# Kernel tuning notes

Measured on AMD Instinct MI355X. Metric: run time of the kernel, lower is better.

## Reference

```python
import jax, jax.numpy as jnp
import numpy as np

B, L = 32, 96
N = B * L
E = B * L * L
HID, LAT, EEMB = 128, 64, 32
NLAYERS = 3
LAMBDA_CONTRAST = 0.05


def _sinusoidal(t, dim):
    half = dim // 2
    freqs = jnp.exp(-jnp.log(10000.0) * jnp.arange(half, dtype=jnp.float32) / (half - 1))
    ang = t[:, None] * freqs[None, :]
    return jnp.concatenate([jnp.sin(ang), jnp.cos(ang)], axis=-1)


def _forward(H_0, X_0, H_1, X_1, cond_embedding, t_graph,
             Wi1, bi1, Wi2, bi2, Wi3, bi3, edge_table,
             We1, be1, We2, be2, Wx, Wh1, bh1, Wh2, bh2, Wout, bout,
             edges, chain_ids, generate_mask, lengths, shift):
    n = H_0.shape[0]
    b = lengths.shape[0]
    batch_ids = jnp.repeat(jnp.arange(b), lengths, total_repeat_length=n)
    t = t_graph[batch_ids]                      # (N,)
    mask = generate_mask
    mask_f = mask.astype(jnp.float32)

    # path interpolation
    tH = t[:, None]
    H_t = jnp.where(mask[:, None], (1.0 - tH) * H_0 + tH * H_1, H_1)
    X_t = jnp.where(mask[:, None], (1.0 - tH) * X_0 + tH * X_1, X_1)
    v_H_target = H_1 - H_0
    v_X_target = X_1 - X_0

    # edge types from chain-id masking (irregular gather)
    row, col = edges[0], edges[1]
    edge_types = (chain_ids[row] != chain_ids[col]).astype(jnp.int32)

    # --- velocity net ---
    t_embed = _sinusoidal(t, HID)
    h = jnp.concatenate([H_t, cond_embedding, t_embed], axis=-1)
    h = jax.nn.relu(h @ Wi1 + bi1)
    h = jax.nn.relu(h @ Wi2 + bi2)
    h = h @ Wi3 + bi3                            # (N, HID)
    eemb = edge_table[edge_types]                # (E, EEMB)

    X = X_t
    for l in range(NLAYERS):
        rel = X[row] - X[col]                    # (E, 3)
        d2 = jnp.sum(rel * rel, axis=-1, keepdims=True)
        ef = jnp.concatenate([h[row], h[col], d2, eemb], axis=-1)
        m = jax.nn.silu(ef @ We1[l] + be1[l])
        m = jax.nn.silu(m @ We2[l] + be2[l])     # (E, HID)
        coef = m @ Wx[l]                         # (E, 1)
        X = X + jax.ops.segment_sum(rel * coef, row, num_segments=n)
        agg = jax.ops.segment_sum(m, row, num_segments=n)
        hh = jnp.concatenate([h, agg], axis=-1)
        h = h + jax.nn.silu(hh @ Wh1[l] + bh1[l]) @ Wh2[l] + bh2[l]

    v_X_pred = jnp.where(mask[:, None], X, 0.0)
    v_H_pred = jnp.where(mask[:, None], h @ Wout + bout, 0.0)

    # --- losses ---
    msum = mask_f.sum() + 1e-8
    def masked_mse(pred, tgt):
        return (jnp.sum((pred - tgt) ** 2, axis=-1) * mask_f).sum() / msum
    loss_H_pos = masked_mse(v_H_pred, v_H_target)
    loss_X_pos = masked_mse(v_X_pred, v_X_target)

    # negatives: roll over node dim (matches torch indexing (arange+shift)%N)
    v_H_target_neg = jnp.roll(H_1, -shift, axis=0) - jnp.roll(H_0, -shift, axis=0)
    v_X_target_neg = jnp.roll(X_1, -shift, axis=0) - jnp.roll(X_0, -shift, axis=0)
    loss_H_neg = masked_mse(v_H_pred, v_H_target_neg)
    loss_X_neg = masked_mse(v_X_pred, v_X_target_neg)

    loss_H = loss_H_pos - LAMBDA_CONTRAST * loss_H_neg
    loss_X = loss_X_pos - LAMBDA_CONTRAST * loss_X_neg
    return jnp.stack([loss_H, loss_X, loss_H_pos, loss_X_pos, loss_H_neg, loss_X_neg])


def setup_inputs() -> dict:
    key = jax.random.key(0)
    ks = iter(jax.random.split(key, 40))
    def nrm(shape, fan_in):
        return jax.random.normal(next(ks), shape, dtype=jnp.float32) / np.sqrt(fan_in)

    # all-pairs edges within each graph (uniform lengths)
    idx = np.arange(L)
    rb, cb = np.repeat(idx, L), np.tile(idx, L)
    off = (np.arange(B) * L)[:, None]
    rows = (off + rb[None, :]).reshape(-1)
    cols = (off + cb[None, :]).reshape(-1)
    edges = jnp.asarray(np.stack([rows, cols]).astype(np.int32))

    d_in_mlp = LAT + 2 * HID       # 320
    d_in_e = 2 * HID + 1 + EEMB    # 289
    inp = {
        "H_0": jax.random.normal(next(ks), (N, LAT), dtype=jnp.float32),
        "X_0": jax.random.normal(next(ks), (N, 3), dtype=jnp.float32),
        "H_1": jax.random.normal(next(ks), (N, LAT), dtype=jnp.float32),
        "X_1": jax.random.normal(next(ks), (N, 3), dtype=jnp.float32),
        "cond_embedding": jax.random.normal(next(ks), (N, HID), dtype=jnp.float32),
        "t_graph": jax.random.uniform(next(ks), (B,), dtype=jnp.float32),
        "Wi1": nrm((d_in_mlp, HID), d_in_mlp), "bi1": jnp.zeros((HID,)),
        "Wi2": nrm((HID, HID), HID), "bi2": jnp.zeros((HID,)),
        "Wi3": nrm((HID, HID), HID), "bi3": jnp.zeros((HID,)),
        "edge_table": jax.random.normal(next(ks), (2, EEMB), dtype=jnp.float32),
        "We1": nrm((NLAYERS, d_in_e, HID), d_in_e), "be1": jnp.zeros((NLAYERS, HID)),
        "We2": nrm((NLAYERS, HID, HID), HID), "be2": jnp.zeros((NLAYERS, HID)),
        "Wx": nrm((NLAYERS, HID, 1), HID) * 0.01,
        "Wh1": nrm((NLAYERS, 2 * HID, HID), 2 * HID), "bh1": jnp.zeros((NLAYERS, HID)),
        "Wh2": nrm((NLAYERS, HID, HID), HID), "bh2": jnp.zeros((NLAYERS, HID)),
        "Wout": nrm((HID, LAT), HID), "bout": jnp.zeros((LAT,)),
        "edges": edges,
        "chain_ids": jax.random.randint(next(ks), (N,), 0, 3).astype(jnp.int32),
        "generate_mask": jax.random.bernoulli(next(ks), 0.5, (N,)),
        "lengths": jnp.full((B,), L, dtype=jnp.int32),
        "shift": 7,
    }
    return inp


def reference(H_0, X_0, H_1, X_1, cond_embedding, t_graph,
              Wi1, bi1, Wi2, bi2, Wi3, bi3, edge_table,
              We1, be1, We2, be2, Wx, Wh1, bh1, Wh2, bh2, Wout, bout,
              edges, chain_ids, generate_mask, lengths, shift):
    return _forward(H_0, X_0, H_1, X_1, cond_embedding, t_graph,
                    Wi1, bi1, Wi2, bi2, Wi3, bi3, edge_table,
                    We1, be1, We2, be2, Wx, Wh1, bh1, Wh2, bh2, Wout, bout,
                    edges, chain_ids, generate_mask, lengths, shift)
```

## Files before the change

kernel.cpp:

```cpp
#include <hip/hip_runtime.h>
#include <hip/hip_bf16.h>
#include <math.h>

#define NBATCH 32
#define LSEQ   96
#define NN     3072
#define HID    128
#define LAT    64
#define EEMB   32

#define OFF_H      0
#define OFF_X      (OFF_H   + NN*HID)
#define OFF_PA     (OFF_X   + NN*3)
#define OFF_AGG    (OFF_PA  + NN*HID)
#define OFF_DX     (OFF_AGG + NN*HID)
#define OFF_ET     (OFF_DX  + NN*3)
#define OFF_ACC    (OFF_ET  + 768)
#define OFF_NBID   (OFF_ACC + 8)
#define OFF_CUM    (OFF_NBID + NN)
#define OFF_PBH    (OFF_CUM + 40)
#define OFF_BPE    (OFF_PBH + NN*HID/2)
#define OFF_BAB    (OFF_BPE + 24576)
#define OFF_BH1    (OFF_BAB + 49152)
#define OFF_BH2    (OFF_BH1 + 49152)
#define OFF_BWO    (OFF_BH2 + 24576)
#define OFF_BWI1   (OFF_BWO + 4096)
#define OFF_BWI2   (OFF_BWI1 + 20480)
#define OFF_BWI3   (OFF_BWI2 + 8192)
#define OFF_CNT    (OFF_BWI3 + 8192)

typedef short bf16x8 __attribute__((ext_vector_type(8)));
typedef float f32x4  __attribute__((ext_vector_type(4)));

__device__ __forceinline__ short f2bf(float f) {
    unsigned u = __builtin_bit_cast(unsigned, f);
    unsigned r = (u + 0x7FFFu + ((u >> 16) & 1u)) >> 16;
    return (short)r;
}
__device__ __forceinline__ short2 f2bf2(float a, float b) {
    __hip_bfloat162 h = __float22bfloat162_rn(make_float2(a, b));
    short2 r;
    __builtin_memcpy(&r, &h, sizeof(r));
    return r;
}
__device__ __forceinline__ float bf2f(short s) {
    unsigned u = ((unsigned)(unsigned short)s) << 16;
    return __builtin_bit_cast(float, u);
}
__device__ __forceinline__ float silu(float z) {
    return z * __builtin_amdgcn_rcpf(1.0f + __expf(-z));
}

__global__ void k0_all(const float* __restrict__ edge_table, const float* __restrict__ We1,
                       const int* __restrict__ lengths, const float* __restrict__ We2,
                       const float* __restrict__ Wh1, const float* __restrict__ Wh2,
                       const float* __restrict__ Wout, const float* __restrict__ Wi1,
                       const float* __restrict__ Wi2, const float* __restrict__ Wi3,
                       float* __restrict__ ws) {
    int tid = threadIdx.x;
    if (blockIdx.x == 1472) {
        int* cum = (int*)(ws + OFF_CUM);
        int* nb  = (int*)(ws + OFF_NBID);
        float* et = ws + OFF_ET;
        if (tid == 0) {
            int s = 0;
            for (int b = 0; b < NBATCH; b++) { cum[b] = s; s += lengths[b]; }
            cum[NBATCH] = s;
        }
        if (tid < 8) ws[OFF_ACC + tid] = 0.0f;
        if (tid < 128) ((unsigned*)(ws + OFF_CNT))[tid] = 0u;
        __syncthreads();
        for (int i = tid; i < NN; i += blockDim.x) {
            int b = NBATCH - 1;
            for (int q = 0; q < NBATCH; q++) { if (i < cum[q + 1]) { b = q; break; } }
            nb[i] = b;
        }
        for (int idx = tid; idx < 3 * 2 * HID; idx += blockDim.x) {
            int c = idx & 127;
            int t = (idx >> 7) & 1;
            int l = idx >> 8;
            const float* w = We1 + (l * 289 + 257) * HID + c;
            const float* e = edge_table + t * EEMB;
            float s = 0.f;
            for (int k = 0; k < EEMB; k++) s += e[k] * w[k * HID];
            et[idx] = s;
        }
        return;
    }
    int idx = blockIdx.x * 256 + tid;
    short* bpe  = (short*)(ws + OFF_BPE);
    short* bab  = (short*)(ws + OFF_BAB);
    short* bh1  = (short*)(ws + OFF_BH1);
    short* bh2  = (short*)(ws + OFF_BH2);
    short* bwo  = (short*)(ws + OFF_BWO);
    short* bwi1 = (short*)(ws + OFF_BWI1);
    short* bwi2 = (short*)(ws + OFF_BWI2);
    short* bwi3 = (short*)(ws + OFF_BWI3);
    if (idx < 49152) {
// ... 129 lines not shown
            acc[i] = __builtin_amdgcn_mfma_f32_16x16x32_bf16(af, bf, acc[i], 0, 0, 0);
        }
    }
    #pragma unroll
    for (int i = 0; i < 2; i++) {
        int ch = 16 * (2 * w + i) + lp;
        float bb2 = bi2[ch];
        #pragma unroll
        for (int r = 0; r < 4; r++)
            u2[(quad * 4 + r) * 136 + ch] = f2bf(fmaxf(acc[i][r] + bb2, 0.0f));
    }
    __syncthreads();

    acc[0] = (f32x4){0.f, 0.f, 0.f, 0.f};
    acc[1] = (f32x4){0.f, 0.f, 0.f, 0.f};
    #pragma unroll
    for (int s = 0; s < 4; s++) {
        int kb = s * 32 + quad * 8;
        bf16x8 af = *(const bf16x8*)(u2 + lp * 136 + kb);
        #pragma unroll
        for (int i = 0; i < 2; i++) {
            int ct = 2 * w + i;
            bf16x8 bf = *(const bf16x8*)(bwi3 + (size_t)(16 * ct + lp) * 128 + kb);
            acc[i] = __builtin_amdgcn_mfma_f32_16x16x32_bf16(af, bf, acc[i], 0, 0, 0);
        }
    }
    #pragma unroll
    for (int i = 0; i < 2; i++) {
        int ch = 16 * (2 * w + i) + lp;
        float bb3 = bi3[ch];
        #pragma unroll
        for (int r = 0; r < 4; r++) {
            int row = quad * 4 + r;
            float h = acc[i][r] + bb3;
            ws[OFF_H + (size_t)(rowbase + row) * 128 + ch] = h;
            u1[row * 136 + ch] = f2bf(h);
        }
    }
    __syncthreads();

    f32x4 acc4[4];
    #pragma unroll
    for (int i = 0; i < 4; i++) acc4[i] = (f32x4){0.f, 0.f, 0.f, 0.f};
    #pragma unroll
    for (int s = 0; s < 4; s++) {
        int kb = s * 32 + quad * 8;
        bf16x8 af = *(const bf16x8*)(u1 + lp * 136 + kb);
        #pragma unroll
        for (int i = 0; i < 4; i++) {
            int ct4 = 4 * w + i;
            bf16x8 bf = *(const bf16x8*)(bab + (size_t)(16 * ct4 + lp) * 128 + kb);
            acc4[i] = __builtin_amdgcn_mfma_f32_16x16x32_bf16(af, bf, acc4[i], 0, 0, 0);
        }
    }
    short* pbh = (short*)(ws + OFF_PBH);
    #pragma unroll
    for (int i = 0; i < 4; i++) {
        int ct4 = 4 * w + i;
        #pragma unroll
        for (int r = 0; r < 4; r++) {
            int node = rowbase + quad * 4 + r;
            if (ct4 < 8) {
                int ch = 16 * ct4 + lp;
                ws[OFF_PA + (size_t)node * 128 + ch] = acc4[i][r] + be1[ch];
            } else {
                int ch = 16 * (ct4 - 8) + lp;
                pbh[(size_t)node * 128 + ch] = f2bf(acc4[i][r]);
            }
        }
    }
}

#define KG 4
#define SMC_BS    0
#define SMC_AGG   32768
#define SMC_PE0   45056
#define SMC_PE1   47104
#define SMC_WC    49152
#define SMC_BE2   49664
#define SMC_WX    50176
#define SMC_COEF  50688
#define SMC_XT    52224
#define SMC_CI    52272
__global__ void __launch_bounds__(384)
k3v_edge(const float* __restrict__ We1, const float* __restrict__ Wx,
         const float* __restrict__ be2, const int* __restrict__ chain,
         int l, float* __restrict__ ws) {
    __shared__ __align__(16) char smem[52288];
    short* bS    = (short*)(smem + SMC_BS);
    float* aggP  = (float*)(smem + SMC_AGG);
    float* pe0S  = (float*)(smem + SMC_PE0);
    float* pe1S  = (float*)(smem + SMC_PE1);
    float* wcS   = (float*)(smem + SMC_WC);
    float* be2S  = (float*)(smem + SMC_BE2);
    float* wxS   = (float*)(smem + SMC_WX);
    float* coefS = (float*)(smem + SMC_COEF);
    float* xT    = (float*)(smem + SMC_XT);
    int*   ciS   = (int*)  (smem + SMC_CI);

    int tid = threadIdx.x;
    int i0 = blockIdx.x * KG;
    int colbase = (i0 / 96) * 96;
    const float* Xc = ws + OFF_X;

    {
        const short* bpe = (const short*)(ws + OFF_BPE) + (size_t)l * 128 * 128;
        for (int idx = tid; idx < 2048; idx += 384) {
            int t = idx >> 8, s = (idx >> 6) & 3, ln = idx & 63;
            int lq = ln >> 4, lpp = ln & 15;
            *(bf16x8*)(bS + idx * 8) =
                *(const bf16x8*)(bpe + (size_t)(16 * t + lpp) * 128 + s * 32 + lq * 8);
        }
        if (tid < 128) {
            float et0 = ws[OFF_ET + l * 256 + tid];
            float et1 = ws[OFF_ET + l * 256 + 128 + tid];
            #pragma unroll
            for (int g = 0; g < KG; g++) {
                float pav = ws[OFF_PA + (size_t)(i0 + g) * 128 + tid];
                pe0S[g * 128 + tid] = pav + et0;
                pe1S[g * 128 + tid] = pav + et1;
            }
            wcS[tid]  = We1[(l * 289 + 256) * 128 + tid];
            be2S[tid] = be2[l * 128 + tid];
            wxS[tid]  = Wx[l * 128 + tid];
        }
        if (tid < KG * 3) xT[tid] = Xc[(size_t)(i0 + tid / 3) * 3 + tid % 3];
        if (tid < KG) ciS[tid] = chain[i0 + tid];
    }

    int w = tid >> 6, lane = tid & 63;
    int quad = lane >> 4, lp = lane & 15;
    int jA = 16 * w + lp;
    const short* pbrow = (const short*)(ws + OFF_PBH) + (size_t)(colbase + jA) * 128;
    float xr0 = Xc[(size_t)(colbase + jA) * 3 + 0];
    float xr1 = Xc[(size_t)(colbase + jA) * 3 + 1];
    float xr2 = Xc[(size_t)(colbase + jA) * 3 + 2];
    int cj = chain[colbase + jA];
    float ex0 = 0.f, ex1 = 0.f;
    if (w < 3) {
        ex0 = Xc[(size_t)(colbase + lane) * 3 + w];
        if (lane < 32) ex1 = Xc[(size_t)(colbase + lane + 64) * 3 + w];
    }
    __syncthreads();

    #pragma unroll
    for (int gr = 0; gr < 2; gr++) {
        int g0 = 2 * gr, g1 = 2 * gr + 1;
        float rx0 = xT[g0 * 3 + 0] - xr0, ry0 = xT[g0 * 3 + 1] - xr1, rz0 = xT[g0 * 3 + 2] - xr2;
        float rx1 = xT[g1 * 3 + 0] - xr0, ry1 = xT[g1 * 3 + 1] - xr1, rz1 = xT[g1 * 3 + 2] - xr2;
        float d20 = rx0 * rx0 + ry0 * ry0 + rz0 * rz0;
        float d21 = rx1 * rx1 + ry1 * ry1 + rz1 * rz1;
        const float* peB0 = ((cj != ciS[g0]) ? pe1S : pe0S) + g0 * 128;
        const float* peB1 = ((cj != ciS[g1]) ? pe1S : pe0S) + g1 * 128;

        bf16x8 af0[4], af1[4];
        #pragma unroll
        for (int s = 0; s < 4; s++) {
            int kb = s * 32 + quad * 8;
            bf16x8 pb = *(const bf16x8*)(pbrow + kb);
            float4 w0 = *(const float4*)(wcS + kb);
            float4 w1 = *(const float4*)(wcS + kb + 4);
            float wcv[8] = {w0.x, w0.y, w0.z, w0.w, w1.x, w1.y, w1.z, w1.w};
            float4 pa0 = *(const float4*)(peB0 + kb);
            float4 pa1 = *(const float4*)(peB0 + kb + 4);
            float4 pb0 = *(const float4*)(peB1 + kb);
            float4 pb1 = *(const float4*)(peB1 + kb + 4);
            float pe0v[8] = {pa0.x, pa0.y, pa0.z, pa0.w, pa1.x, pa1.y, pa1.z, pa1.w};
            float pe1v[8] = {pb0.x, pb0.y, pb0.z, pb0.w, pb1.x, pb1.y, pb1.z, pb1.w};
            float z0[8], z1[8];
            #pragma unroll
            for (int e = 0; e < 8; e++) {
                float pbf = bf2f(pb[e]);
                z0[e] = silu(pe0v[e] + pbf + d20 * wcv[e]);
                z1[e] = silu(pe1v[e] + pbf + d21 * wcv[e]);
            }
            #pragma unroll
            for (int e = 0; e < 8; e += 2) {
                short2 p0 = f2bf2(z0[e], z0[e + 1]);
                short2 p1 = f2bf2(z1[e], z1[e + 1]);
                af0[s][e] = p0.x; af0[s][e + 1] = p0.y;
                af1[s][e] = p1.x; af1[s][e + 1] = p1.y;
            }
        }

        float cp0[4] = {0.f, 0.f, 0.f, 0.f};
        float cp1[4] = {0.f, 0.f, 0.f, 0.f};
        #pragma unroll
        for (int t = 0; t < 8; t++) {
            f32x4 a0 = (f32x4){0.f, 0.f, 0.f, 0.f};
            f32x4 a1 = (f32x4){0.f, 0.f, 0.f, 0.f};
            #pragma unroll
            for (int s = 0; s < 4; s++) {
                bf16x8 bf = *(const bf16x8*)(bS + ((t * 4 + s) * 64 + lane) * 8);
                a0 = __builtin_amdgcn_mfma_f32_16x16x32_bf16(af0[s], bf, a0, 0, 0, 0);
                a1 = __builtin_amdgcn_mfma_f32_16x16x32_bf16(af1[s], bf, a1, 0, 0, 0);
            }
            float be2v = be2S[16 * t + lp];
            float wxv  = wxS[16 * t + lp];
            float ag0 = 0.f, ag1 = 0.f;
            #pragma unroll
            for (int r = 0; r < 4; r++) {
                float m20 = silu(a0[r] + be2v);
                float m21 = silu(a1[r] + be2v);
                ag0 += m20; ag1 += m21;
                cp0[r] += m20 * wxv;
                cp1[r] += m21 * wxv;
            }
            ag0 += __shfl_xor(ag0, 16); ag0 += __shfl_xor(ag0, 32);
            ag1 += __shfl_xor(ag1, 16); ag1 += __shfl_xor(ag1, 32);
            if (lane < 16) {
                aggP[(g0 * 6 + w) * 128 + 16 * t + lp] = ag0;
                aggP[(g1 * 6 + w) * 128 + 16 * t + lp] = ag1;
            }
        }
        #pragma unroll
        for (int r = 0; r < 4; r++) {
            float v0 = cp0[r], v1 = cp1[r];
            v0 += __shfl_xor(v0, 1); v1 += __shfl_xor(v1, 1);
            v0 += __shfl_xor(v0, 2); v1 += __shfl_xor(v1, 2);
            v0 += __shfl_xor(v0, 4); v1 += __shfl_xor(v1, 4);
            v0 += __shfl_xor(v0, 8); v1 += __shfl_xor(v1, 8);
            if (lp == 0) {
                coefS[g0 * 96 + 16 * w + quad * 4 + r] = v0;
                coefS[g1 * 96 + 16 * w + quad * 4 + r] = v1;
            }
        }
        __syncthreads();

        if (tid < 256) {
            int gg = tid >> 7, ch = tid & 127;
            int g = 2 * gr + gg;
            float s = 0.f;
            #pragma unroll
            for (int q = 0; q < 6; q++) s += aggP[(g * 6 + q) * 128 + ch];
            ws[OFF_AGG + (size_t)(i0 + g) * 128 + ch] = s;
        }
        if (w < 3) {
            #pragma unroll
            for (int gg = 0; gg < 2; gg++) {
                int g = 2 * gr + gg;
                float v = (xT[g * 3 + w] - ex0) * coefS[g * 96 + lane];
                if (lane < 32) v += (xT[g * 3 + w] - ex1) * coefS[g * 96 + lane + 64];
                #pragma unroll
                for (int o = 32; o > 0; o >>= 1) v += __shfl_down(v, o);
                if (lane == 0) ws[OFF_DX + (size_t)(i0 + g) * 3 + w] = v;
            }
        }
    }
}

__global__ void __launch_bounds__(256)
k4s_node_post(const float* __restrict__ bh1, const float* __restrict__ bh2,
              const float* __restrict__ be1, const float* __restrict__ bout,
              const float* __restrict__ H0, const float* __restrict__ X0,
              const float* __restrict__ H1, const float* __restrict__ X1,
              const int* __restrict__ gmask, const int* __restrict__ shiftp,
              int l, float* __restrict__ ws, float* __restrict__ out) {
    __shared__ short uS[16 * 136];
    __shared__ short hS[16 * 136];
    __shared__ float redE[4], redN[4];
    __shared__ float sxp, sxn, scnt;
    int rowbase = blockIdx.x * 96 + blockIdx.y * 16;
    int tid = threadIdx.x;
    int w = tid >> 6, lane = tid & 63;
    int quad = lane >> 4, lp = lane & 15;
    int nodeA = rowbase + lp;
    const short* b1 = (const short*)(ws + OFF_BH1) + (size_t)l * 128 * 256;
    const short* b2 = (const short*)(ws + OFF_BH2) + (size_t)l * 128 * 128;

    if (tid == 0) { sxp = 0.f; sxn = 0.f; scnt = 0.f; }
    if (tid < 48) {
        int node = rowbase + tid / 3, d = tid % 3;
        ws[OFF_X + (size_t)node * 3 + d] += ws[OFF_DX + (size_t)node * 3 + d];
    }

    f32x4 acc[2];
    acc[0] = (f32x4){0.f, 0.f, 0.f, 0.f};
    acc[1] = (f32x4){0.f, 0.f, 0.f, 0.f};
    #pragma unroll
    for (int s = 0; s < 8; s++) {
        int kb = s * 32 + quad * 8;
        const float* src = (kb < 128) ? (ws + OFF_H + (size_t)nodeA * 128 + kb)
                                      : (ws + OFF_AGG + (size_t)nodeA * 128 + (kb - 128));
        bf16x8 af;
        #pragma unroll
        for (int e = 0; e < 8; e += 2) {
            short2 p = f2bf2(src[e], src[e + 1]);
            af[e] = p.x; af[e + 1] = p.y;
        }
        #pragma unroll
        for (int i = 0; i < 2; i++) {
            int ct = 2 * w + i;
            bf16x8 bf = *(const bf16x8*)(b1 + (size_t)(16 * ct + lp) * 256 + kb);
            acc[i] = __builtin_amdgcn_mfma_f32_16x16x32_bf16(af, bf, acc[i], 0, 0, 0);
        }
    }
    #pragma unroll
    for (int i = 0; i < 2; i++) {
        int ch = 16 * (2 * w + i) + lp;
        float bb1 = bh1[l * 128 + ch];
        #pragma unroll
        for (int r = 0; r < 4; r++)
            uS[(quad * 4 + r) * 136 + ch] = f2bf(silu(acc[i][r] + bb1));
    }
    __syncthreads();

    acc[0] = (f32x4){0.f, 0.f, 0.f, 0.f};
    acc[1] = (f32x4){0.f, 0.f, 0.f, 0.f};
    #pragma unroll
    for (int s = 0; s < 4; s++) {
        int kb = s * 32 + quad * 8;
        bf16x8 af = *(const bf16x8*)(uS + lp * 136 + kb);
        #pragma unroll
        for (int i = 0; i < 2; i++) {
            int ct = 2 * w + i;
            bf16x8 bf = *(const bf16x8*)(b2 + (size_t)(16 * ct + lp) * 128 + kb);
            acc[i] = __builtin_amdgcn_mfma_f32_16x16x32_bf16(af, bf, acc[i], 0, 0, 0);
        }
    }
    #pragma unroll
    for (int i = 0; i < 2; i++) {
        int ch = 16 * (2 * w + i) + lp;
        float bb2 = bh2[l * 128 + ch];
        #pragma unroll
        for (int r = 0; r < 4; r++) {
            int row = quad * 4 + r;
            size_t off = OFF_H + (size_t)(rowbase + row) * 128 + ch;
            float h = ws[off] + acc[i][r] + bb2;
            ws[off] = h;
            hS[row * 136 + ch] = f2bf(h);
        }
    }
    __syncthreads();

    if (l < 2) {
        const short* bab = (const short*)(ws + OFF_BAB) + (size_t)(l + 1) * 256 * 128;
        f32x4 acc4[4];
        #pragma unroll
        for (int i = 0; i < 4; i++) acc4[i] = (f32x4){0.f, 0.f, 0.f, 0.f};
        #pragma unroll
        for (int s = 0; s < 4; s++) {
            int kb = s * 32 + quad * 8;
            bf16x8 af = *(const bf16x8*)(hS + lp * 136 + kb);
            #pragma unroll
            for (int i = 0; i < 4; i++) {
                int ct4 = 4 * w + i;
                bf16x8 bf = *(const bf16x8*)(bab + (size_t)(16 * ct4 + lp) * 128 + kb);
                acc4[i] = __builtin_amdgcn_mfma_f32_16x16x32_bf16(af, bf, acc4[i], 0, 0, 0);
            }
        }
        short* pbh = (short*)(ws + OFF_PBH);
        #pragma unroll
        for (int i = 0; i < 4; i++) {
            int ct4 = 4 * w + i;
            #pragma unroll
            for (int r = 0; r < 4; r++) {
                int node = rowbase + quad * 4 + r;
                if (ct4 < 8) {
                    int ch = 16 * ct4 + lp;
                    ws[OFF_PA + (size_t)node * 128 + ch] = acc4[i][r] + be1[(l + 1) * 128 + ch];
                } else {
                    int ch = 16 * (ct4 - 8) + lp;
                    pbh[(size_t)node * 128 + ch] = f2bf(acc4[i][r]);
                }
            }
        }
    } else {
        const short* bwo = (const short*)(ws + OFF_BWO);
        f32x4 accv = (f32x4){0.f, 0.f, 0.f, 0.f};
        #pragma unroll
        for (int s = 0; s < 4; s++) {
            int kb = s * 32 + quad * 8;
            bf16x8 af = *(const bf16x8*)(hS + lp * 136 + kb);
            bf16x8 bf = *(const bf16x8*)(bwo + (size_t)(16 * w + lp) * 128 + kb);
            accv = __builtin_amdgcn_mfma_f32_16x16x32_bf16(af, bf, accv, 0, 0, 0);
        }
        int s = shiftp[0] % NN; if (s < 0) s += NN;
        int col = 16 * w + lp;
        float bo = bout[col];
        float ep = 0.f, en = 0.f;
        #pragma unroll
        for (int r = 0; r < 4; r++) {
            int row = rowbase + quad * 4 + r;
            if (gmask[row] != 0) {
                int ip = row + s; if (ip >= NN) ip -= NN;
                float v  = accv[r] + bo;
                float tp = H1[(size_t)row * 64 + col] - H0[(size_t)row * 64 + col];
                float tn = H1[(size_t)ip * 64 + col]  - H0[(size_t)ip * 64 + col];
                float dp = v - tp, dn = v - tn;
                ep += dp * dp;
                en += dn * dn;
            }
        }
        #pragma unroll
        for (int o = 1; o < 64; o <<= 1) {
            ep += __shfl_xor(ep, o);
            en += __shfl_xor(en, o);
        }
        if (lane == 0) { redE[w] = ep; redN[w] = en; }

        if (tid < 16) {
            int node = rowbase + tid;
            if (gmask[node] != 0) {
                int ip = node + s; if (ip >= NN) ip -= NN;
                float xp = 0.f, xn = 0.f;
                #pragma unroll
                for (int d = 0; d < 3; d++) {
                    float xv  = ws[OFF_X + (size_t)node * 3 + d];
                    float tpx = X1[(size_t)node * 3 + d] - X0[(size_t)node * 3 + d];
                    float tnx = X1[(size_t)ip * 3 + d]   - X0[(size_t)ip * 3 + d];
                    xp += (xv - tpx) * (xv - tpx);
                    xn += (xv - tnx) * (xv - tnx);
                }
                atomicAdd(&sxp, xp);
                atomicAdd(&sxn, xn);
                atomicAdd(&scnt, 1.0f);
            }
        }
        __syncthreads();
        if (tid == 0) {
            float eT = redE[0] + redE[1] + redE[2] + redE[3];
            float nT = redN[0] + redN[1] + redN[2] + redN[3];
            float* acc0 = ws + OFF_ACC;
            atomicAdd(acc0 + 0, eT);
            atomicAdd(acc0 + 2, nT);
            atomicAdd(acc0 + 1, sxp);
            atomicAdd(acc0 + 3, sxn);
            atomicAdd(acc0 + 4, scnt);
            __threadfence();
            unsigned o2 = atomicAdd((unsigned*)(ws + OFF_CNT) + 96, 1u);
            if (o2 == 191u) {
                __threadfence();
                float a0 = atomicAdd(acc0 + 0, 0.0f);
                float a1 = atomicAdd(acc0 + 1, 0.0f);
                float a2 = atomicAdd(acc0 + 2, 0.0f);
                float a3 = atomicAdd(acc0 + 3, 0.0f);
                float a4 = atomicAdd(acc0 + 4, 0.0f);
                float msum = a4 + 1e-8f;
                float lhp = a0 / msum, lxp = a1 / msum;
                float lhn = a2 / msum, lxn = a3 / msum;
                out[0] = lhp - 0.05f * lhn;
                out[1] = lxp - 0.05f * lxn;
                out[2] = lhp;
                out[3] = lxp;
                out[4] = lhn;
                out[5] = lxn;
            }
        }
    }
}

extern "C" void kernel_launch(void* const* d_in, const int* in_sizes, int n_in,
                              void* d_out, int out_size, void* d_ws, size_t ws_size,
                              hipStream_t stream) {
    (void)in_sizes; (void)n_in; (void)out_size; (void)ws_size;
    const float* H0   = (const float*)d_in[0];
    const float* X0   = (const float*)d_in[1];
    const float* H1   = (const float*)d_in[2];
    const float* X1   = (const float*)d_in[3];
    const float* cond = (const float*)d_in[4];
    const float* tg   = (const float*)d_in[5];
    const float* Wi1  = (const float*)d_in[6];
    const float* bi1  = (const float*)d_in[7];
    const float* Wi2  = (const float*)d_in[8];
    const float* bi2  = (const float*)d_in[9];
    const float* Wi3  = (const float*)d_in[10];
    const float* bi3  = (const float*)d_in[11];
    const float* etab = (const float*)d_in[12];
    const float* We1  = (const float*)d_in[13];
    const float* be1  = (const float*)d_in[14];
    const float* We2  = (const float*)d_in[15];
    const float* be2  = (const float*)d_in[16];
    const float* Wx   = (const float*)d_in[17];
    const float* Wh1  = (const float*)d_in[18];
    const float* bh1  = (const float*)d_in[19];
    const float* Wh2  = (const float*)d_in[20];
    const float* bh2  = (const float*)d_in[21];
    const float* Wout = (const float*)d_in[22];
    const float* bout = (const float*)d_in[23];
    const int* chain   = (const int*)d_in[25];
    const int* gmask   = (const int*)d_in[26];
    const int* lengths = (const int*)d_in[27];
    const int* shiftp  = (const int*)d_in[28];
    float* ws  = (float*)d_ws;
    float* out = (float*)d_out;

    k0_all<<<1473, 256, 0, stream>>>(etab, We1, lengths, We2, Wh1, Wh2,
                                     Wout, Wi1, Wi2, Wi3, ws);
    k1s_node_init<<<dim3(NBATCH, 6), 256, 0, stream>>>(H0, X0, H1, X1, cond, tg,
                                                       bi1, bi2, bi3, be1, gmask, ws);
    for (int l = 0; l < 3; l++) {
        k3v_edge<<<NN / KG, 384, 0, stream>>>(We1, Wx, be2, chain, l, ws);
        k4s_node_post<<<dim3(NBATCH, 6), 256, 0, stream>>>(bh1, bh2, be1, bout,
                                                           H0, X0, H1, X1, gmask, shiftp,
                                                           l, ws, out);
    }
}
```

Baseline: 353.5 us.

## Fuse edge message kernel with node update via ping-pong X and PBH buffers

Merges the per-layer edge kernel and the node post-processing kernel into one launch. Each 4-node block now reduces its aggregated messages in shared memory, applies the node MLP, and writes the next layer's projections itself. This removes the global agg buffer round trip and one launch per layer. Double-buffered X and bf16 projection buffers keep other blocks from reading values that are being overwritten. The cost is that node-MLP MFMAs use 16-row tiles with only 4 valid rows, and each of four times as many blocks re-reads the node weight matrices.

```diff
diff --git a/kernel.cpp b/kernel.cpp
--- a/kernel.cpp
+++ b/kernel.cpp
@@ -12,8 +12,8 @@
 #define OFF_H      0
 #define OFF_X      (OFF_H   + NN*HID)
 #define OFF_PA     (OFF_X   + NN*3)
-#define OFF_AGG    (OFF_PA  + NN*HID)
-#define OFF_DX     (OFF_AGG + NN*HID)
+#define OFF_PBH2   (OFF_PA  + NN*HID)
+#define OFF_DX     (OFF_PBH2 + NN*HID)
 #define OFF_ET     (OFF_DX  + NN*3)
 #define OFF_ACC    (OFF_ET  + 768)
 #define OFF_NBID   (OFF_ACC + 8)
@@ -309,11 +309,17 @@
 #define SMC_COEF  50688
 #define SMC_XT    52224
 #define SMC_CI    52272
+#define SMC_XN    52288
 __global__ void __launch_bounds__(384)
-k3v_edge(const float* __restrict__ We1, const float* __restrict__ Wx,
-         const float* __restrict__ be2, const int* __restrict__ chain,
-         int l, float* __restrict__ ws) {
-    __shared__ __align__(16) char smem[52288];
+k3f_edge_node(const float* __restrict__ We1, const float* __restrict__ Wx,
+              const float* __restrict__ be2, const int* __restrict__ chain,
+              const float* __restrict__ bh1, const float* __restrict__ bh2,
+              const float* __restrict__ be1, const float* __restrict__ bout,
+              const float* __restrict__ H0, const float* __restrict__ X0,
+              const float* __restrict__ H1, const float* __restrict__ X1,
+              const int* __restrict__ gmask, const int* __restrict__ shiftp,
+              int l, float* __restrict__ ws, float* __restrict__ out) {
+    __shared__ __align__(16) char smem[52336];
     short* bS    = (short*)(smem + SMC_BS);
     float* aggP  = (float*)(smem + SMC_AGG);
     float* pe0S  = (float*)(smem + SMC_PE0);
@@ -324,11 +330,15 @@
     float* coefS = (float*)(smem + SMC_COEF);
     float* xT    = (float*)(smem + SMC_XT);
     int*   ciS   = (int*)  (smem + SMC_CI);
+    float* xnS   = (float*)(smem + SMC_XN);
 
     int tid = threadIdx.x;
     int i0 = blockIdx.x * KG;
     int colbase = (i0 / 96) * 96;
-    const float* Xc = ws + OFF_X;
+    const float* Xin  = ws + ((l & 1) ? OFF_DX : OFF_X);
+    float*       Xout = ws + ((l & 1) ? OFF_X  : OFF_DX);
+    const short* pbh_in  = (const short*)(ws + ((l & 1) ? OFF_PBH2 : OFF_PBH));
+    short*       pbh_out = (short*)      (ws + ((l & 1) ? OFF_PBH  : OFF_PBH2));
 
     {
         const short* bpe = (const short*)(ws + OFF_BPE) + (size_t)l * 128 * 128;
@@ -351,22 +361,22 @@
             be2S[tid] = be2[l * 128 + tid];
             wxS[tid]  = Wx[l * 128 + tid];
         }
-        if (tid < KG * 3) xT[tid] = Xc[(size_t)(i0 + tid / 3) * 3 + tid % 3];
+        if (tid < KG * 3) xT[tid] = Xin[(size_t)(i0 + tid / 3) * 3 + tid % 3];
         if (tid < KG) ciS[tid] = chain[i0 + tid];
     }
 
     int w = tid >> 6, lane = tid & 63;
     int quad = lane >> 4, lp = lane & 15;
     int jA = 16 * w + lp;
-    const short* pbrow = (const short*)(ws + OFF_PBH) + (size_t)(colbase + jA) * 128;
-    float xr0 = Xc[(size_t)(colbase + jA) * 3 + 0];
-    float xr1 = Xc[(size_t)(colbase + jA) * 3 + 1];
-    float xr2 = Xc[(size_t)(colbase + jA) * 3 + 2];
+    const short* pbrow = pbh_in + (size_t)(colbase + jA) * 128;
+    float xr0 = Xin[(size_t)(colbase + jA) * 3 + 0];
+    float xr1 = Xin[(size_t)(colbase + jA) * 3 + 1];
+    float xr2 = Xin[(size_t)(colbase + jA) * 3 + 2];
     int cj = chain[colbase + jA];
     float ex0 = 0.f, ex1 = 0.f;
     if (w < 3) {
-        ex0 = Xc[(size_t)(colbase + lane) * 3 + w];
-        if (lane < 32) ex1 = Xc[(size_t)(colbase + lane + 64) * 3 + w];
+        ex0 = Xin[(size_t)(colbase + lane) * 3 + w];
+        if (lane < 32) ex1 = Xin[(size_t)(colbase + lane + 64) * 3 + w];
     }
     __syncthreads();
 
@@ -454,14 +464,6 @@
         }
         __syncthreads();
 
-        if (tid < 256) {
-            int gg = tid >> 7, ch = tid & 127;
-            int g = 2 * gr + gg;
-            float s = 0.f;
-            #pragma unroll
-            for (int q = 0; q < 6; q++) s += aggP[(g * 6 + q) * 128 + ch];
-            ws[OFF_AGG + (size_t)(i0 + g) * 128 + ch] = s;
-        }
         if (w < 3) {
             #pragma unroll
             for (int gg = 0; gg < 2; gg++) {
@@ -470,193 +472,180 @@
                 if (lane < 32) v += (xT[g * 3 + w] - ex1) * coefS[g * 96 + lane + 64];
                 #pragma unroll
                 for (int o = 32; o > 0; o >>= 1) v += __shfl_down(v, o);
-                if (lane == 0) ws[OFF_DX + (size_t)(i0 + g) * 3 + w] = v;
-            }
-        }
-    }
-}
-
-__global__ void __launch_bounds__(256)
-k4s_node_post(const float* __restrict__ bh1, const float* __restrict__ bh2,
-              const float* __restrict__ be1, const float* __restrict__ bout,
-              const float* __restrict__ H0, const float* __restrict__ X0,
-              const float* __restrict__ H1, const float* __restrict__ X1,
-              const int* __restrict__ gmask, const int* __restrict__ shiftp,
-              int l, float* __restrict__ ws, float* __restrict__ out) {
-    __shared__ short uS[16 * 136];
-    __shared__ short hS[16 * 136];
-    __shared__ float redE[4], redN[4];
-    __shared__ float sxp, sxn, scnt;
-    int rowbase = blockIdx.x * 96 + blockIdx.y * 16;
-    int tid = threadIdx.x;
-    int w = tid >> 6, lane = tid & 63;
-    int quad = lane >> 4, lp = lane & 15;
-    int nodeA = rowbase + lp;
-    const short* b1 = (const short*)(ws + OFF_BH1) + (size_t)l * 128 * 256;
-    const short* b2 = (const short*)(ws + OFF_BH2) + (size_t)l * 128 * 128;
-
-    if (tid == 0) { sxp = 0.f; sxn = 0.f; scnt = 0.f; }
-    if (tid < 48) {
-        int node = rowbase + tid / 3, d = tid % 3;
-        ws[OFF_X + (size_t)node * 3 + d] += ws[OFF_DX + (size_t)node * 3 + d];
-    }
-
-    f32x4 acc[2];
-    acc[0] = (f32x4){0.f, 0.f, 0.f, 0.f};
-    acc[1] = (f32x4){0.f, 0.f, 0.f, 0.f};
-    #pragma unroll
-    for (int s = 0; s < 8; s++) {
-        int kb = s * 32 + quad * 8;
-        const float* src = (kb < 128) ? (ws + OFF_H + (size_t)nodeA * 128 + kb)
-                                      : (ws + OFF_AGG + (size_t)nodeA * 128 + (kb - 128));
-        bf16x8 af;
-        #pragma unroll
-        for (int e = 0; e < 8; e += 2) {
-            short2 p = f2bf2(src[e], src[e + 1]);
-            af[e] = p.x; af[e + 1] = p.y;
-        }
-        #pragma unroll
-        for (int i = 0; i < 2; i++) {
-            int ct = 2 * w + i;
-            bf16x8 bf = *(const bf16x8*)(b1 + (size_t)(16 * ct + lp) * 256 + kb);
-            acc[i] = __builtin_amdgcn_mfma_f32_16x16x32_bf16(af, bf, acc[i], 0, 0, 0);
-        }
-    }
-    #pragma unroll
-    for (int i = 0; i < 2; i++) {
-        int ch = 16 * (2 * w + i) + lp;
-        float bb1 = bh1[l * 128 + ch];
-        #pragma unroll
-        for (int r = 0; r < 4; r++)
-            uS[(quad * 4 + r) * 136 + ch] = f2bf(silu(acc[i][r] + bb1));
-    }
+                if (lane == 0) {
+                    float xv = xT[g * 3 + w] + v;
+                    Xout[(size_t)(i0 + g) * 3 + w] = xv;
+                    xnS[g * 3 + w] = xv;
+                }
+            }
+        }
+    }
+
+    short* haggS = (short*)(smem + SMC_PE0);
+    short* uS    = (short*)(smem + SMC_COEF);
+    short* hS    = (short*)(smem + SMC_PE1);
+    const bf16x8 zf = (bf16x8){0, 0, 0, 0, 0, 0, 0, 0};
+
+    for (int idx = tid; idx < 1024; idx += 384) {
+        int g = idx >> 8, c = idx & 255;
+        float v;
+        if (c < 128) {
+            v = ws[OFF_H + (size_t)(i0 + g) * 128 + c];
+        } else {
+            int ch = c - 128;
+            v = 0.f;
+            #pragma unroll
+            for (int q = 0; q < 6; q++) v += aggP[(g * 6 + q) * 128 + ch];
+        }
+        haggS[g * 256 + c] = f2bf(v);
+    }
+    if (l == 2 && tid < 16) ((float*)(smem + SMC_WX))[tid] = 0.f;
     __syncthreads();
 
-    acc[0] = (f32x4){0.f, 0.f, 0.f, 0.f};
-    acc[1] = (f32x4){0.f, 0.f, 0.f, 0.f};
-    #pragma unroll
-    for (int s = 0; s < 4; s++) {
-        int kb = s * 32 + quad * 8;
-        bf16x8 af = *(const bf16x8*)(uS + lp * 136 + kb);
-        #pragma unroll
-        for (int i = 0; i < 2; i++) {
-            int ct = 2 * w + i;
-            bf16x8 bf = *(const bf16x8*)(b2 + (size_t)(16 * ct + lp) * 128 + kb);
-            acc[i] = __builtin_amdgcn_mfma_f32_16x16x32_bf16(af, bf, acc[i], 0, 0, 0);
-        }
-    }
-    #pragma unroll
-    for (int i = 0; i < 2; i++) {
-        int ch = 16 * (2 * w + i) + lp;
-        float bb2 = bh2[l * 128 + ch];
-        #pragma unroll
-        for (int r = 0; r < 4; r++) {
-            int row = quad * 4 + r;
-            size_t off = OFF_H + (size_t)(rowbase + row) * 128 + ch;
-            float h = ws[off] + acc[i][r] + bb2;
-            ws[off] = h;
-            hS[row * 136 + ch] = f2bf(h);
+    {
+        const short* b1 = (const short*)(ws + OFF_BH1) + (size_t)l * 128 * 256;
+        for (int ct = w; ct < 8; ct += 6) {
+            f32x4 acc = (f32x4){0.f, 0.f, 0.f, 0.f};
+            #pragma unroll
+            for (int s = 0; s < 8; s++) {
+                int kb = s * 32 + quad * 8;
+                bf16x8 af = zf;
+                if (lp < 4) af = *(const bf16x8*)(haggS + lp * 256 + kb);
+                bf16x8 bf = *(const bf16x8*)(b1 + (size_t)(16 * ct + lp) * 256 + kb);
+                acc = __builtin_amdgcn_mfma_f32_16x16x32_bf16(af, bf, acc, 0, 0, 0);
+            }
+            if (quad == 0) {
+                int ch = 16 * ct + lp;
+                float bb = bh1[l * 128 + ch];
+                #pragma unroll
+                for (int r = 0; r < 4; r++)
+                    uS[r * 136 + ch] = f2bf(silu(acc[r] + bb));
+            }
+        }
+    }
+    __syncthreads();
+
+    {
+        const short* b2 = (const short*)(ws + OFF_BH2) + (size_t)l * 128 * 128;
+        for (int ct = w; ct < 8; ct += 6) {
+            f32x4 acc = (f32x4){0.f, 0.f, 0.f, 0.f};
+            #pragma unroll
+            for (int s = 0; s < 4; s++) {
+                int kb = s * 32 + quad * 8;
+                bf16x8 af = zf;
+                if (lp < 4) af = *(const bf16x8*)(uS + lp * 136 + kb);
+                bf16x8 bf = *(const bf16x8*)(b2 + (size_t)(16 * ct + lp) * 128 + kb);
+                acc = __builtin_amdgcn_mfma_f32_16x16x32_bf16(af, bf, acc, 0, 0, 0);
+            }
+            if (quad == 0) {
+                int ch = 16 * ct + lp;
+                float bb = bh2[l * 128 + ch];
+                #pragma unroll
+                for (int r = 0; r < 4; r++) {
+                    size_t off = OFF_H + (size_t)(i0 + r) * 128 + ch;
+                    float h = ws[off] + acc[r] + bb;
+                    ws[off] = h;
+                    hS[r * 136 + ch] = f2bf(h);
+                }
+            }
         }
     }
     __syncthreads();
 
     if (l < 2) {
         const short* bab = (const short*)(ws + OFF_BAB) + (size_t)(l + 1) * 256 * 128;
-        f32x4 acc4[4];
-        #pragma unroll
-        for (int i = 0; i < 4; i++) acc4[i] = (f32x4){0.f, 0.f, 0.f, 0.f};
-        #pragma unroll
-        for (int s = 0; s < 4; s++) {
-            int kb = s * 32 + quad * 8;
-            bf16x8 af = *(const bf16x8*)(hS + lp * 136 + kb);
-            #pragma unroll
-            for (int i = 0; i < 4; i++) {
-                int ct4 = 4 * w + i;
+        for (int ct4 = w; ct4 < 16; ct4 += 6) {
+            f32x4 acc = (f32x4){0.f, 0.f, 0.f, 0.f};
+            #pragma unroll
+            for (int s = 0; s < 4; s++) {
+                int kb = s * 32 + quad * 8;
+                bf16x8 af = zf;
+                if (lp < 4) af = *(const bf16x8*)(hS + lp * 136 + kb);
                 bf16x8 bf = *(const bf16x8*)(bab + (size_t)(16 * ct4 + lp) * 128 + kb);
-                acc4[i] = __builtin_amdgcn_mfma_f32_16x16x32_bf16(af, bf, acc4[i], 0, 0, 0);
-            }
-        }
-        short* pbh = (short*)(ws + OFF_PBH);
-        #pragma unroll
-        for (int i = 0; i < 4; i++) {
-            int ct4 = 4 * w + i;
-            #pragma unroll
-            for (int r = 0; r < 4; r++) {
-                int node = rowbase + quad * 4 + r;
-                if (ct4 < 8) {
-                    int ch = 16 * ct4 + lp;
-                    ws[OFF_PA + (size_t)node * 128 + ch] = acc4[i][r] + be1[(l + 1) * 128 + ch];
-                } else {
-                    int ch = 16 * (ct4 - 8) + lp;
-                    pbh[(size_t)node * 128 + ch] = f2bf(acc4[i][r]);
+                acc = __builtin_amdgcn_mfma_f32_16x16x32_bf16(af, bf, acc, 0, 0, 0);
+            }
+            if (quad == 0) {
+                #pragma unroll
+                for (int r = 0; r < 4; r++) {
+                    int node = i0 + r;
+                    if (ct4 < 8) {
+                        int ch = 16 * ct4 + lp;
+                        ws[OFF_PA + (size_t)node * 128 + ch] = acc[r] + be1[(l + 1) * 128 + ch];
+                    } else {
+                        int ch = 16 * (ct4 - 8) + lp;
+                        pbh_out[(size_t)node * 128 + ch] = f2bf(acc[r]);
+                    }
                 }
             }
         }
     } else {
+        float* redS = (float*)(smem + SMC_WX);
         const short* bwo = (const short*)(ws + OFF_BWO);
         f32x4 accv = (f32x4){0.f, 0.f, 0.f, 0.f};
-        #pragma unroll
-        for (int s = 0; s < 4; s++) {
-            int kb = s * 32 + quad * 8;
-            bf16x8 af = *(const bf16x8*)(hS + lp * 136 + kb);
-            bf16x8 bf = *(const bf16x8*)(bwo + (size_t)(16 * w + lp) * 128 + kb);
-            accv = __builtin_amdgcn_mfma_f32_16x16x32_bf16(af, bf, accv, 0, 0, 0);
-        }
-        int s = shiftp[0] % NN; if (s < 0) s += NN;
-        int col = 16 * w + lp;
-        float bo = bout[col];
+        bool act = (w < 4);
+        if (act) {
+            #pragma unroll
+            for (int s = 0; s < 4; s++) {
+                int kb = s * 32 + quad * 8;
+                bf16x8 af = zf;
+                if (lp < 4) af = *(const bf16x8*)(hS + lp * 136 + kb);
+                bf16x8 bf = *(const bf16x8*)(bwo + (size_t)(16 * w + lp) * 128 + kb);
+                accv = __builtin_amdgcn_mfma_f32_16x16x32_bf16(af, bf, accv, 0, 0, 0);
+            }
+        }
+        int sft = shiftp[0] % NN; if (sft < 0) sft += NN;
         float ep = 0.f, en = 0.f;
-        #pragma unroll
-        for (int r = 0; r < 4; r++) {
-            int row = rowbase + quad * 4 + r;
-            if (gmask[row] != 0) {
-                int ip = row + s; if (ip >= NN) ip -= NN;
-                float v  = accv[r] + bo;
-                float tp = H1[(size_t)row * 64 + col] - H0[(size_t)row * 64 + col];
-                float tn = H1[(size_t)ip * 64 + col]  - H0[(size_t)ip * 64 + col];
-                float dp = v - tp, dn = v - tn;
-                ep += dp * dp;
-                en += dn * dn;
-            }
-        }
-        #pragma unroll
-        for (int o = 1; o < 64; o <<= 1) {
-            ep += __shfl_xor(ep, o);
-            en += __shfl_xor(en, o);
-        }
-        if (lane == 0) { redE[w] = ep; redN[w] = en; }
-
-        if (tid < 16) {
-            int node = rowbase + tid;
+        if (act && quad == 0) {
+            int col = 16 * w + lp;
+            float bo = bout[col];
+            #pragma unroll
+            for (int r = 0; r < 4; r++) {
+                int node = i0 + r;
+                if (gmask[node] != 0) {
+                    int ip = node + sft; if (ip >= NN) ip -= NN;
+                    float v  = accv[r] + bo;
+                    float tp = H1[(size_t)node * 64 + col] - H0[(size_t)node * 64 + col];
+                    float tn = H1[(size_t)ip * 64 + col]  - H0[(size_t)ip * 64 + col];
+                    float dp = v - tp, dn = v - tn;
+                    ep += dp * dp;
+                    en += dn * dn;
+                }
+            }
+        }
+        ep += __shfl_xor(ep, 1); en += __shfl_xor(en, 1);
+        ep += __shfl_xor(ep, 2); en += __shfl_xor(en, 2);
+        ep += __shfl_xor(ep, 4); en += __shfl_xor(en, 4);
+        ep += __shfl_xor(ep, 8); en += __shfl_xor(en, 8);
+        if (act && lane == 0) { redS[w] = ep; redS[4 + w] = en; }
+
+        if (tid < 12) {
+            int g = tid / 3, d = tid % 3;
+            int node = i0 + g;
             if (gmask[node] != 0) {
-                int ip = node + s; if (ip >= NN) ip -= NN;
-                float xp = 0.f, xn = 0.f;
-                #pragma unroll
-                for (int d = 0; d < 3; d++) {
-                    float xv  = ws[OFF_X + (size_t)node * 3 + d];
-                    float tpx = X1[(size_t)node * 3 + d] - X0[(size_t)node * 3 + d];
-                    float tnx = X1[(size_t)ip * 3 + d]   - X0[(size_t)ip * 3 + d];
-                    xp += (xv - tpx) * (xv - tpx);
-                    xn += (xv - tnx) * (xv - tnx);
-                }
-                atomicAdd(&sxp, xp);
-                atomicAdd(&sxn, xn);
-                atomicAdd(&scnt, 1.0f);
-            }
+                int ip = node + sft; if (ip >= NN) ip -= NN;
+                float xv  = xnS[g * 3 + d];
+                float tpx = X1[(size_t)node * 3 + d] - X0[(size_t)node * 3 + d];
+                float tnx = X1[(size_t)ip * 3 + d]   - X0[(size_t)ip * 3 + d];
+                atomicAdd(&redS[8], (xv - tpx) * (xv - tpx));
+                atomicAdd(&redS[9], (xv - tnx) * (xv - tnx));
+            }
+        }
+        if (tid < 4) {
+            if (gmask[i0 + tid] != 0) atomicAdd(&redS[10], 1.0f);
         }
         __syncthreads();
         if (tid == 0) {
-            float eT = redE[0] + redE[1] + redE[2] + redE[3];
-            float nT = redN[0] + redN[1] + redN[2] + redN[3];
+            float eT = redS[0] + redS[1] + redS[2] + redS[3];
+            float nT = redS[4] + redS[5] + redS[6] + redS[7];
             float* acc0 = ws + OFF_ACC;
             atomicAdd(acc0 + 0, eT);
             atomicAdd(acc0 + 2, nT);
-            atomicAdd(acc0 + 1, sxp);
-            atomicAdd(acc0 + 3, sxn);
-            atomicAdd(acc0 + 4, scnt);
+            atomicAdd(acc0 + 1, redS[8]);
+            atomicAdd(acc0 + 3, redS[9]);
+            atomicAdd(acc0 + 4, redS[10]);
             __threadfence();
             unsigned o2 = atomicAdd((unsigned*)(ws + OFF_CNT) + 96, 1u);
-            if (o2 == 191u) {
+            if (o2 == 767u) {
                 __threadfence();
                 float a0 = atomicAdd(acc0 + 0, 0.0f);
                 float a1 = atomicAdd(acc0 + 1, 0.0f);
@@ -717,9 +706,9 @@
     k1s_node_init<<<dim3(NBATCH, 6), 256, 0, stream>>>(H0, X0, H1, X1, cond, tg,
                                                        bi1, bi2, bi3, be1, gmask, ws);
     for (int l = 0; l < 3; l++) {
-        k3v_edge<<<NN / KG, 384, 0, stream>>>(We1, Wx, be2, chain, l, ws);
-        k4s_node_post<<<dim3(NBATCH, 6), 256, 0, stream>>>(bh1, bh2, be1, bout,
-                                                           H0, X0, H1, X1, gmask, shiftp,
-                                                           l, ws, out);
+        k3f_edge_node<<<NN / KG, 384, 0, stream>>>(We1, Wx, be2, chain,
+                                                   bh1, bh2, be1, bout,
+                                                   H0, X0, H1, X1, gmask, shiftp,
+                                                   l, ws, out);
     }
 }
```

After: 413.0 us. +16.8%, slower.

## Split node-post kernel into 8-row blocks with 512 threads and staged inputs

Applied to the files above, without the earlier changes.

The node update kernel now processes 8 nodes per block with 8 waves, giving 384 blocks instead of 192. Each wave owns one 16-column output tile, and the concatenated h/agg input is staged once into shared memory as bf16 using vectorized float4 loads. MFMA tiles are half-padded with zero rows, so half of the matrix compute is wasted in exchange for more parallelism across CUs. The loss-completion counter threshold is updated to 383, and a __syncthreads is added inside the edge kernel loop.

```diff
diff --git a/kernel.cpp b/kernel.cpp
--- a/kernel.cpp
+++ b/kernel.cpp
@@ -473,150 +473,154 @@
                 if (lane == 0) ws[OFF_DX + (size_t)(i0 + g) * 3 + w] = v;
             }
         }
-    }
-}
-
-__global__ void __launch_bounds__(256)
+        __syncthreads();
+    }
+}
+
+__global__ void __launch_bounds__(512)
 k4s_node_post(const float* __restrict__ bh1, const float* __restrict__ bh2,
               const float* __restrict__ be1, const float* __restrict__ bout,
               const float* __restrict__ H0, const float* __restrict__ X0,
               const float* __restrict__ H1, const float* __restrict__ X1,
               const int* __restrict__ gmask, const int* __restrict__ shiftp,
               int l, float* __restrict__ ws, float* __restrict__ out) {
-    __shared__ short uS[16 * 136];
-    __shared__ short hS[16 * 136];
+    __shared__ short haggS[8 * 264];
+    __shared__ short uS[8 * 136];
+    __shared__ short hS[8 * 136];
     __shared__ float redE[4], redN[4];
     __shared__ float sxp, sxn, scnt;
-    int rowbase = blockIdx.x * 96 + blockIdx.y * 16;
+    int rowbase = blockIdx.x * 96 + blockIdx.y * 8;
     int tid = threadIdx.x;
     int w = tid >> 6, lane = tid & 63;
     int quad = lane >> 4, lp = lane & 15;
-    int nodeA = rowbase + lp;
     const short* b1 = (const short*)(ws + OFF_BH1) + (size_t)l * 128 * 256;
     const short* b2 = (const short*)(ws + OFF_BH2) + (size_t)l * 128 * 128;
+    const bf16x8 zf = (bf16x8){0, 0, 0, 0, 0, 0, 0, 0};
 
     if (tid == 0) { sxp = 0.f; sxn = 0.f; scnt = 0.f; }
-    if (tid < 48) {
+    if (tid < 24) {
         int node = rowbase + tid / 3, d = tid % 3;
         ws[OFF_X + (size_t)node * 3 + d] += ws[OFF_DX + (size_t)node * 3 + d];
     }
-
-    f32x4 acc[2];
-    acc[0] = (f32x4){0.f, 0.f, 0.f, 0.f};
-    acc[1] = (f32x4){0.f, 0.f, 0.f, 0.f};
-    #pragma unroll
-    for (int s = 0; s < 8; s++) {
-        int kb = s * 32 + quad * 8;
-        const float* src = (kb < 128) ? (ws + OFF_H + (size_t)nodeA * 128 + kb)
-                                      : (ws + OFF_AGG + (size_t)nodeA * 128 + (kb - 128));
-        bf16x8 af;
-        #pragma unroll
-        for (int e = 0; e < 8; e += 2) {
-            short2 p = f2bf2(src[e], src[e + 1]);
-            af[e] = p.x; af[e + 1] = p.y;
-        }
-        #pragma unroll
-        for (int i = 0; i < 2; i++) {
-            int ct = 2 * w + i;
-            bf16x8 bf = *(const bf16x8*)(b1 + (size_t)(16 * ct + lp) * 256 + kb);
-            acc[i] = __builtin_amdgcn_mfma_f32_16x16x32_bf16(af, bf, acc[i], 0, 0, 0);
-        }
-    }
-    #pragma unroll
-    for (int i = 0; i < 2; i++) {
-        int ch = 16 * (2 * w + i) + lp;
-        float bb1 = bh1[l * 128 + ch];
-        #pragma unroll
-        for (int r = 0; r < 4; r++)
-            uS[(quad * 4 + r) * 136 + ch] = f2bf(silu(acc[i][r] + bb1));
+    {
+        int g = tid >> 6;
+        int c = (tid & 63) * 4;
+        const float* src = (c < 128)
+            ? (ws + OFF_H   + (size_t)(rowbase + g) * 128 + c)
+            : (ws + OFF_AGG + (size_t)(rowbase + g) * 128 + (c - 128));
+        float4 v = *(const float4*)src;
+        haggS[g * 264 + c + 0] = f2bf(v.x);
+        haggS[g * 264 + c + 1] = f2bf(v.y);
+        haggS[g * 264 + c + 2] = f2bf(v.z);
+        haggS[g * 264 + c + 3] = f2bf(v.w);
     }
     __syncthreads();
 
-    acc[0] = (f32x4){0.f, 0.f, 0.f, 0.f};
-    acc[1] = (f32x4){0.f, 0.f, 0.f, 0.f};
-    #pragma unroll
-    for (int s = 0; s < 4; s++) {
-        int kb = s * 32 + quad * 8;
-        bf16x8 af = *(const bf16x8*)(uS + lp * 136 + kb);
-        #pragma unroll
-        for (int i = 0; i < 2; i++) {
-            int ct = 2 * w + i;
-            bf16x8 bf = *(const bf16x8*)(b2 + (size_t)(16 * ct + lp) * 128 + kb);
-            acc[i] = __builtin_amdgcn_mfma_f32_16x16x32_bf16(af, bf, acc[i], 0, 0, 0);
-        }
-    }
-    #pragma unroll
-    for (int i = 0; i < 2; i++) {
-        int ch = 16 * (2 * w + i) + lp;
-        float bb2 = bh2[l * 128 + ch];
-        #pragma unroll
-        for (int r = 0; r < 4; r++) {
-            int row = quad * 4 + r;
-            size_t off = OFF_H + (size_t)(rowbase + row) * 128 + ch;
-            float h = ws[off] + acc[i][r] + bb2;
-            ws[off] = h;
-            hS[row * 136 + ch] = f2bf(h);
+    {
+        f32x4 acc = (f32x4){0.f, 0.f, 0.f, 0.f};
+        #pragma unroll
+        for (int s = 0; s < 8; s++) {
+            int kb = s * 32 + quad * 8;
+            bf16x8 af = zf;
+            if (lp < 8) af = *(const bf16x8*)(haggS + lp * 264 + kb);
+            bf16x8 bf = *(const bf16x8*)(b1 + (size_t)(16 * w + lp) * 256 + kb);
+            acc = __builtin_amdgcn_mfma_f32_16x16x32_bf16(af, bf, acc, 0, 0, 0);
+        }
+        if (quad < 2) {
+            int ch = 16 * w + lp;
+            float bb = bh1[l * 128 + ch];
+            #pragma unroll
+            for (int r = 0; r < 4; r++)
+                uS[(quad * 4 + r) * 136 + ch] = f2bf(silu(acc[r] + bb));
+        }
+    }
+    __syncthreads();
+
+    {
+        f32x4 acc = (f32x4){0.f, 0.f, 0.f, 0.f};
+        #pragma unroll
+        for (int s = 0; s < 4; s++) {
+            int kb = s * 32 + quad * 8;
+            bf16x8 af = zf;
+            if (lp < 8) af = *(const bf16x8*)(uS + lp * 136 + kb);
+            bf16x8 bf = *(const bf16x8*)(b2 + (size_t)(16 * w + lp) * 128 + kb);
+            acc = __builtin_amdgcn_mfma_f32_16x16x32_bf16(af, bf, acc, 0, 0, 0);
+        }
+        if (quad < 2) {
+            int ch = 16 * w + lp;
+            float bb = bh2[l * 128 + ch];
+            #pragma unroll
+            for (int r = 0; r < 4; r++) {
+                int row = quad * 4 + r;
+                size_t off = OFF_H + (size_t)(rowbase + row) * 128 + ch;
+                float h = ws[off] + acc[r] + bb;
+                ws[off] = h;
+                hS[row * 136 + ch] = f2bf(h);
+            }
         }
     }
     __syncthreads();
 
     if (l < 2) {
         const short* bab = (const short*)(ws + OFF_BAB) + (size_t)(l + 1) * 256 * 128;
-        f32x4 acc4[4];
-        #pragma unroll
-        for (int i = 0; i < 4; i++) acc4[i] = (f32x4){0.f, 0.f, 0.f, 0.f};
-        #pragma unroll
-        for (int s = 0; s < 4; s++) {
-            int kb = s * 32 + quad * 8;
-            bf16x8 af = *(const bf16x8*)(hS + lp * 136 + kb);
-            #pragma unroll
-            for (int i = 0; i < 4; i++) {
-                int ct4 = 4 * w + i;
+        short* pbh = (short*)(ws + OFF_PBH);
+        #pragma unroll
+        for (int i = 0; i < 2; i++) {
+            int ct4 = w + 8 * i;
+            f32x4 acc = (f32x4){0.f, 0.f, 0.f, 0.f};
+            #pragma unroll
+            for (int s = 0; s < 4; s++) {
+                int kb = s * 32 + quad * 8;
+                bf16x8 af = zf;
+                if (lp < 8) af = *(const bf16x8*)(hS + lp * 136 + kb);
                 bf16x8 bf = *(const bf16x8*)(bab + (size_t)(16 * ct4 + lp) * 128 + kb);
-                acc4[i] = __builtin_amdgcn_mfma_f32_16x16x32_bf16(af, bf, acc4[i], 0, 0, 0);
-            }
-        }
-        short* pbh = (short*)(ws + OFF_PBH);
-        #pragma unroll
-        for (int i = 0; i < 4; i++) {
-            int ct4 = 4 * w + i;
-            #pragma unroll
-            for (int r = 0; r < 4; r++) {
-                int node = rowbase + quad * 4 + r;
-                if (ct4 < 8) {
-                    int ch = 16 * ct4 + lp;
-                    ws[OFF_PA + (size_t)node * 128 + ch] = acc4[i][r] + be1[(l + 1) * 128 + ch];
-                } else {
-                    int ch = 16 * (ct4 - 8) + lp;
-                    pbh[(size_t)node * 128 + ch] = f2bf(acc4[i][r]);
+                acc = __builtin_amdgcn_mfma_f32_16x16x32_bf16(af, bf, acc, 0, 0, 0);
+            }
+            if (quad < 2) {
+                #pragma unroll
+                for (int r = 0; r < 4; r++) {
+                    int node = rowbase + quad * 4 + r;
+                    if (ct4 < 8) {
+                        int ch = 16 * ct4 + lp;
+                        ws[OFF_PA + (size_t)node * 128 + ch] = acc[r] + be1[(l + 1) * 128 + ch];
+                    } else {
+                        int ch = 16 * (ct4 - 8) + lp;
+                        pbh[(size_t)node * 128 + ch] = f2bf(acc[r]);
+                    }
                 }
             }
         }
     } else {
         const short* bwo = (const short*)(ws + OFF_BWO);
         f32x4 accv = (f32x4){0.f, 0.f, 0.f, 0.f};
-        #pragma unroll
-        for (int s = 0; s < 4; s++) {
-            int kb = s * 32 + quad * 8;
-            bf16x8 af = *(const bf16x8*)(hS + lp * 136 + kb);
-            bf16x8 bf = *(const bf16x8*)(bwo + (size_t)(16 * w + lp) * 128 + kb);
-            accv = __builtin_amdgcn_mfma_f32_16x16x32_bf16(af, bf, accv, 0, 0, 0);
-        }
-        int s = shiftp[0] % NN; if (s < 0) s += NN;
-        int col = 16 * w + lp;
-        float bo = bout[col];
+        bool act = (w < 4);
+        if (act) {
+            #pragma unroll
+            for (int s = 0; s < 4; s++) {
+                int kb = s * 32 + quad * 8;
+                bf16x8 af = zf;
+                if (lp < 8) af = *(const bf16x8*)(hS + lp * 136 + kb);
+                bf16x8 bf = *(const bf16x8*)(bwo + (size_t)(16 * w + lp) * 128 + kb);
+                accv = __builtin_amdgcn_mfma_f32_16x16x32_bf16(af, bf, accv, 0, 0, 0);
+            }
+        }
+        int sft = shiftp[0] % NN; if (sft < 0) sft += NN;
         float ep = 0.f, en = 0.f;
-        #pragma unroll
-        for (int r = 0; r < 4; r++) {
-            int row = rowbase + quad * 4 + r;
-            if (gmask[row] != 0) {
-                int ip = row + s; if (ip >= NN) ip -= NN;
-                float v  = accv[r] + bo;
-                float tp = H1[(size_t)row * 64 + col] - H0[(size_t)row * 64 + col];
-                float tn = H1[(size_t)ip * 64 + col]  - H0[(size_t)ip * 64 + col];
-                float dp = v - tp, dn = v - tn;
-                ep += dp * dp;
-                en += dn * dn;
+        if (act && quad < 2) {
+            int col = 16 * w + lp;
+            float bo = bout[col];
+            #pragma unroll
+            for (int r = 0; r < 4; r++) {
+                int node = rowbase + quad * 4 + r;
+                if (gmask[node] != 0) {
+                    int ip = node + sft; if (ip >= NN) ip -= NN;
+                    float v  = accv[r] + bo;
+                    float tp = H1[(size_t)node * 64 + col] - H0[(size_t)node * 64 + col];
+                    float tn = H1[(size_t)ip * 64 + col]  - H0[(size_t)ip * 64 + col];
+                    float dp = v - tp, dn = v - tn;
+                    ep += dp * dp;
+                    en += dn * dn;
+                }
             }
         }
         #pragma unroll
@@ -624,12 +628,12 @@
             ep += __shfl_xor(ep, o);
             en += __shfl_xor(en, o);
         }
-        if (lane == 0) { redE[w] = ep; redN[w] = en; }
-
-        if (tid < 16) {
+        if (act && lane == 0) { redE[w] = ep; redN[w] = en; }
+
+        if (tid < 8) {
             int node = rowbase + tid;
             if (gmask[node] != 0) {
-                int ip = node + s; if (ip >= NN) ip -= NN;
+                int ip = node + sft; if (ip >= NN) ip -= NN;
                 float xp = 0.f, xn = 0.f;
                 #pragma unroll
                 for (int d = 0; d < 3; d++) {
@@ -656,7 +660,7 @@
             atomicAdd(acc0 + 4, scnt);
             __threadfence();
             unsigned o2 = atomicAdd((unsigned*)(ws + OFF_CNT) + 96, 1u);
-            if (o2 == 191u) {
+            if (o2 == 383u) {
                 __threadfence();
                 float a0 = atomicAdd(acc0 + 0, 0.0f);
                 float a1 = atomicAdd(acc0 + 1, 0.0f);
@@ -718,8 +722,8 @@
                                                        bi1, bi2, bi3, be1, gmask, ws);
     for (int l = 0; l < 3; l++) {
         k3v_edge<<<NN / KG, 384, 0, stream>>>(We1, Wx, be2, chain, l, ws);
-        k4s_node_post<<<dim3(NBATCH, 6), 256, 0, stream>>>(bh1, bh2, be1, bout,
-                                                           H0, X0, H1, X1, gmask, shiftp,
-                                                           l, ws, out);
-    }
-}
+        k4s_node_post<<<dim3(NBATCH, 12), 512, 0, stream>>>(bh1, bh2, be1, bout,
+                                                            H0, X0, H1, X1, gmask, shiftp,
+                                                            l, ws, out);
+    }
+}
```

Result: slower. 378.2 us (+7.0%).
